# Kernel tuning notes

Measured on AMD Instinct MI355X. Metric: run time of the kernel, lower is better.

## Reference

```python
import jax, jax.numpy as jnp
import numpy as np

B, S, D, H, DFF = 2, 2048, 512, 8, 2048
DH = D // H
EPS = 1e-5


def setup_inputs() -> dict:
    key = jax.random.key(0)
    ks = jax.random.split(key, 12)
    g = lambda k, shape, s=0.02: jax.random.normal(k, shape, dtype=jnp.float32) * s
    x = jax.random.normal(ks[0], (B, S, D), dtype=jnp.float32)
    # additive causal mask: 0 on/below diag, -inf above
    neg = jnp.finfo(jnp.float32).min
    attn_mask = jnp.where(jnp.tril(jnp.ones((S, S), dtype=bool)), 0.0, neg).astype(jnp.float32)
    return {
        "x": x,
        "attn_mask": attn_mask,
        "Wq": g(ks[1], (D, D)), "bq": jnp.zeros((D,), jnp.float32),
        "Wk": g(ks[2], (D, D)), "bk": jnp.zeros((D,), jnp.float32),
        "Wv": g(ks[3], (D, D)), "bv": jnp.zeros((D,), jnp.float32),
        "Wo": g(ks[4], (D, D)), "bo": jnp.zeros((D,), jnp.float32),
        "head_alphas": jnp.ones((H,), jnp.float32),
        "ln1_g": jnp.ones((D,), jnp.float32), "ln1_b": jnp.zeros((D,), jnp.float32),
        "W1": g(ks[5], (DFF, D)), "b1": jnp.zeros((DFF,), jnp.float32),
        "W2": g(ks[6], (D, DFF)), "b2": jnp.zeros((D,), jnp.float32),
        "ln2_g": jnp.ones((D,), jnp.float32), "ln2_b": jnp.zeros((D,), jnp.float32),
    }


def _layer_norm(h, g, b):
    mu = jnp.mean(h, axis=-1, keepdims=True)
    var = jnp.mean((h - mu) ** 2, axis=-1, keepdims=True)
    return (h - mu) * jax.lax.rsqrt(var + EPS) * g + b


def reference(x, attn_mask, Wq, bq, Wk, bk, Wv, bv, Wo, bo, head_alphas,
              ln1_g, ln1_b, W1, b1, W2, b2, ln2_g, ln2_b):
    scale = jnp.sqrt(jnp.asarray(DH, dtype=x.dtype))
    # projections (torch Linear: x @ W.T + b)
    q = (x @ Wq.T + bq).reshape(B, S, H, DH).transpose(0, 2, 1, 3)  # bhsd
    k = (x @ Wk.T + bk).reshape(B, S, H, DH).transpose(0, 2, 1, 3)
    v = (x @ Wv.T + bv).reshape(B, S, H, DH).transpose(0, 2, 1, 3)
    attn = jnp.einsum('bhqd,bhkd->bhqk', q, k) / scale
    attn = attn + attn_mask  # broadcast [S,S] over batch/heads
    attn = jax.nn.softmax(attn, axis=-1)
    ctx = jnp.einsum('bhqk,bhkd->bhqd', attn, v)
    ctx = ctx * head_alphas[None, :, None, None]
    ctx = ctx.transpose(0, 2, 1, 3).reshape(B, S, D)
    attn_out = ctx @ Wo.T + bo
    # residual + LN
    h = _layer_norm(x + attn_out, ln1_g, ln1_b)
    # FFN (linear -> ReLU -> linear), residual + LN
    ff = jax.nn.relu(h @ W1.T + b1) @ W2.T + b2
    out = _layer_norm(h + ff, ln2_g, ln2_b)
    return out
```

## Files before the change

### kernel.cpp

```cpp
#include <hip/hip_runtime.h>
#include <hip/hip_bf16.h>
#include <math.h>

#define BB 2
#define SS 2048
#define DD 512
#define HH 8
#define DH 64
#define DFF 2048
#define MM (BB*SS)
#define EPS 1e-5f

typedef __attribute__((ext_vector_type(8))) short bf16x8;
typedef __attribute__((ext_vector_type(4))) float f32x4;

#define GL2LDS(g, l)                                                        \
    __builtin_amdgcn_global_load_lds(                                       \
        (const __attribute__((address_space(1))) void*)(unsigned long long)(g), \
        (__attribute__((address_space(3))) void*)(unsigned int)(unsigned long long)(l), \
        16, 0, 0)

struct Cvt7 {
    const float* s[7];
    unsigned short* d[7];
    unsigned off[8];
};

__global__ __launch_bounds__(256) void cvt_k(Cvt7 a)
{
    unsigned i = blockIdx.x * 256 + threadIdx.x;
    int seg = 0;
    #pragma unroll
    for (int t = 1; t < 7; ++t) seg += (i >= a.off[t]);
    unsigned li = i - a.off[seg];
    float4 v = ((const float4*)a.s[seg])[li];
    union { __hip_bfloat16 h[4]; uint2 u; } t;
    t.h[0] = __float2bfloat16(v.x);
    t.h[1] = __float2bfloat16(v.y);
    t.h[2] = __float2bfloat16(v.z);
    t.h[3] = __float2bfloat16(v.w);
    ((uint2*)a.d[seg])[li] = t.u;
}

template<int TM, int TN>
static __device__ __forceinline__ void gemm_core(
    __hip_bfloat16* As, __hip_bfloat16* Bs,
    const __hip_bfloat16* __restrict__ A, const __hip_bfloat16* __restrict__ Bw,
    const float* __restrict__ bias, const float* __restrict__ resid,
    void* __restrict__ Cout, int N_, int K_, int mode, float oscale)
{
    const int tid   = threadIdx.x;
    const int w     = tid >> 6;
    const int lane  = tid & 63;
    const int quad  = lane >> 4;
    const int col16 = lane & 15;
    const int m0 = blockIdx.y * TM;
    const int n0 = blockIdx.x * TN;
    constexpr int MI = TM / 32;
    constexpr int NJ = TN / 32;
    const int wm = (w >> 1) * (TM / 2);
    const int wn = (w & 1) * (TN / 2);

    const int srow = lane >> 3;
    const int scol = (lane & 7) * 8;
    constexpr int CH_A  = TM / 8;
    constexpr int CH_T  = (TM + TN) / 8;
    constexpr int TPW   = CH_T / 4;

    f32x4 acc[MI][NJ] = {};

    for (int k0 = 0; k0 < K_; k0 += 64) {
        __syncthreads();
        #pragma unroll
        for (int t = 0; t < TPW; ++t) {
            const int c = w * TPW + t;
            if (c < CH_A) {
                GL2LDS(A  + (size_t)(m0 + c*8 + srow) * K_ + k0 + scol,
                       (char*)As + c * 1024);
            } else {
                const int cb = c - CH_A;
                GL2LDS(Bw + (size_t)(n0 + cb*8 + srow) * K_ + k0 + scol,
                       (char*)Bs + cb * 1024);
            }
        }
        __syncthreads();

        #pragma unroll
        for (int kk = 0; kk < 64; kk += 32) {
            bf16x8 af[MI], bf[NJ];
            #pragma unroll
            for (int i = 0; i < MI; ++i)
                af[i] = *(const bf16x8*)(As + (wm + i*16 + col16) * 64 + kk + quad*8);
            #pragma unroll
            for (int j = 0; j < NJ; ++j)
                bf[j] = *(const bf16x8*)(Bs + (wn + j*16 + col16) * 64 + kk + quad*8);
            #pragma unroll
            for (int i = 0; i < MI; ++i)
                #pragma unroll
                for (int j = 0; j < NJ; ++j)
                    acc[i][j] = __builtin_amdgcn_mfma_f32_16x16x32_bf16(
                        af[i], bf[j], acc[i][j], 0, 0, 0);
        }
    }

    #pragma unroll
    for (int i = 0; i < MI; ++i) {
        #pragma unroll
        for (int r = 0; r < 4; ++r) {
            const int m = m0 + wm + i*16 + quad*4 + r;
            #pragma unroll
            for (int j = 0; j < NJ; ++j) {
                const int n = n0 + wn + j*16 + col16;
                float vv = acc[i][j][r] + bias[n];
                if (mode == 0) {
                    size_t idx = (size_t)m * N_ + n;
                    float* Cf = (float*)Cout;
                    if (resid) vv += resid[idx];
                    Cf[idx] = vv;
                } else if (mode == 3) {
                    ((__hip_bfloat16*)Cout)[(size_t)m * N_ + n] =
                        __float2bfloat16(fmaxf(vv, 0.f));
                } else {
                    const int b = m >> 11, s = m & (SS - 1);
                    const int hh = n >> 6, d = n & (DH - 1);
                    if (mode == 1)
                        ((__hip_bfloat16*)Cout)[(((size_t)(b*HH + hh))*SS + s)*DH + d] =
                            __float2bfloat16(vv * oscale);
                    else
                        ((__hip_bfloat16*)Cout)[(((size_t)(b*HH + hh))*DH + d)*SS + s] =
                            __float2bfloat16(vv);
                }
            }
        }
    }
}

__global__ __launch_bounds__(256) void gemm128_k(
    const __hip_bfloat16* __restrict__ A, const __hip_bfloat16* __restrict__ Bw,
    const float* __restrict__ bias, const float* __restrict__ resid,
    void* __restrict__ Cout, int N_, int K_, int mode, float oscale)
{
    __shared__ __hip_bfloat16 As[128*64];
    __shared__ __hip_bfloat16 Bs[128*64];
    gemm_core<128,128>(As, Bs, A, Bw, bias, resid, Cout, N_, K_, mode, oscale);
}

__global__ __launch_bounds__(256) void gemm64_k(
    const __hip_bfloat16* __restrict__ A, const __hip_bfloat16* __restrict__ Bw,
    const float* __restrict__ bias, const float* __restrict__ resid,
    void* __restrict__ Cout, int N_, int K_, int mode, float oscale)
{
    __shared__ __hip_bfloat16 As[64*64];
    __shared__ __hip_bfloat16 Bs[64*64];
    gemm_core<64,64>(As, Bs, A, Bw, bias, resid, Cout, N_, K_, mode, oscale);
}

__global__ __launch_bounds__(256) void qkv_mfma_k(
    const __hip_bfloat16* __restrict__ xb,
    const __hip_bfloat16* __restrict__ Wqb, const __hip_bfloat16* __restrict__ Wkb,
    const __hip_bfloat16* __restrict__ Wvb,
    const float* __restrict__ bq, const float* __restrict__ bk,
    const float* __restrict__ bv,
    __hip_bfloat16* __restrict__ qb, __hip_bfloat16* __restrict__ kb,
    __hip_bfloat16* __restrict__ vtb)
{
    __shared__ __hip_bfloat16 As[64*64];
    __shared__ __hip_bfloat16 Bs[64*64];
    const int z = blockIdx.z;
    const __hip_bfloat16* W = (z == 0) ? Wqb : (z == 1) ? Wkb : Wvb;
    const float* bia        = (z == 0) ? bq  : (z == 1) ? bk  : bv;
    void* dst               = (z == 0) ? (void*)qb : (z == 1) ? (void*)kb : (void*)vtb;
    const int mode          = (z == 2) ? 2 : 1;
    const float sc          = (z == 0) ? 0.125f : 1.0f;
    gemm_core<64,64>(As, Bs, xb, W, bia, nullptr, dst, DD, DD, mode, sc);
}

__global__ __launch_bounds__(256) void attn_mfma_k(
    const __hip_bfloat16* __restrict__ Q,
    const __hip_bfloat16* __restrict__ K,
    const __hip_bfloat16* __restrict__ VT,
    const float* __restrict__ halpha,
    __hip_bfloat16* __restrict__ ctx)
{
    const int w    = threadIdx.x >> 6;
    const int lane = threadIdx.x & 63;
    const int quad = lane >> 4;
    const int col  = lane & 15;
    const int bh   = blockIdx.x;
    const int b    = bh >> 3, h = bh & 7;
    const int qt   = gridDim.y - 1 - blockIdx.y;
    const int q0   = qt * 16;
    const int cd   = q0 >> 6;
    const int nchunk = cd + 1;

    const __hip_bfloat16* Qbh = Q  + (size_t)bh * SS * DH;
    const __hip_bfloat16* Kbh = K  + (size_t)bh * SS * DH;
    const __hip_bfloat16* Vbh = VT + (size_t)bh * DH * SS;

    __shared__ __hip_bfloat16 p_lds[4][2][64][8];
    __shared__ float o_lds[4][16][68];
    __shared__ float l_lds[4][16];

    bf16x8 qf0 = *(const bf16x8*)(Qbh + (size_t)(q0 + col) * DH + quad * 8);
    bf16x8 qf1 = *(const bf16x8*)(Qbh + (size_t)(q0 + col) * DH + 32 + quad * 8);

    f32x4 acc_o[4] = {};
    float lp[4] = {0.f, 0.f, 0.f, 0.f};

    for (int c = w; c < nchunk; c += 4) {
        const int k0 = c * 64;

        f32x4 sacc[4];
        #pragma unroll
        for (int ks = 0; ks < 4; ++ks) {
            const __hip_bfloat16* kp = Kbh + (size_t)(k0 + ks*16 + col) * DH + quad * 8;
            bf16x8 kb0 = *(const bf16x8*)(kp);
            bf16x8 kb1 = *(const bf16x8*)(kp + 32);
            f32x4 z = {};
            z = __builtin_amdgcn_mfma_f32_16x16x32_bf16(qf0, kb0, z, 0, 0, 0);
            z = __builtin_amdgcn_mfma_f32_16x16x32_bf16(qf1, kb1, z, 0, 0, 0);
            sacc[ks] = z;
        }

        float pv[4][4];
        if (c == cd) {
            #pragma unroll
            for (int ks = 0; ks < 4; ++ks) {
                int kg = k0 + ks*16 + col;
                #pragma unroll
                for (int r = 0; r < 4; ++r) {
                    int qg = q0 + quad*4 + r;
                    pv[ks][r] = (kg > qg) ? 0.f : __expf(sacc[ks][r]);
                }
            }
        } else {
            #pragma unroll
            for (int ks = 0; ks < 4; ++ks)
                #pragma unroll
                for (int r = 0; r < 4; ++r)
                    pv[ks][r] = __expf(sacc[ks][r]);
        }
        #pragma unroll
        for (int r = 0; r < 4; ++r)
            lp[r] += (pv[0][r] + pv[1][r]) + (pv[2][r] + pv[3][r]);

        #pragma unroll
        for (int ks = 0; ks < 4; ++ks) {
            int keyl = ks*16 + col;
            int kh = keyl >> 5;
            int lr = ((keyl >> 3) & 3) * 16;
            int j  = keyl & 7;
            #pragma unroll
            for (int r = 0; r < 4; ++r)
                p_lds[w][kh][lr + quad*4 + r][j] = __float2bfloat16(pv[ks][r]);
        }

        bf16x8 pa0 = *(const bf16x8*)&p_lds[w][0][lane][0];
        bf16x8 pa1 = *(const bf16x8*)&p_lds[w][1][lane][0];
        #pragma unroll
        for (int d = 0; d < 4; ++d) {
            const __hip_bfloat16* vp = Vbh + (size_t)(d*16 + col) * SS + k0 + quad * 8;
            bf16x8 vb0 = *(const bf16x8*)(vp);
            bf16x8 vb1 = *(const bf16x8*)(vp + 32);
            acc_o[d] = __builtin_amdgcn_mfma_f32_16x16x32_bf16(pa0, vb0, acc_o[d], 0, 0, 0);
            acc_o[d] = __builtin_amdgcn_mfma_f32_16x16x32_bf16(pa1, vb1, acc_o[d], 0, 0, 0);
        }
    }

    #pragma unroll
    for (int r = 0; r < 4; ++r) {
        float s_ = lp[r];
        #pragma unroll
        for (int o = 1; o < 16; o <<= 1) s_ += __shfl_xor(s_, o);
        lp[r] = s_;
    }

    if (col == 0) {
        #pragma unroll
        for (int r = 0; r < 4; ++r) l_lds[w][quad*4 + r] = lp[r];
    }
    #pragma unroll
    for (int d = 0; d < 4; ++d)
        #pragma unroll
        for (int r = 0; r < 4; ++r)
            o_lds[w][quad*4 + r][d*16 + col] = acc_o[d][r];
    __syncthreads();

    const float ha = halpha[h];
    #pragma unroll
    for (int r = 0; r < 4; ++r) {
        const int row = quad*4 + r;
        float L = (l_lds[0][row] + l_lds[1][row]) + (l_lds[2][row] + l_lds[3][row]);
        float val = (o_lds[0][row][w*16+col] + o_lds[1][row][w*16+col])
                  + (o_lds[2][row][w*16+col] + o_lds[3][row][w*16+col]);
        ctx[((size_t)(b*SS + q0 + row))*DD + h*64 + w*16 + col] =
            __float2bfloat16(val * ha / L);
    }
}

__global__ __launch_bounds__(256) void ln_k(
    const float* __restrict__ in, const float* __restrict__ g,
    const float* __restrict__ bta, float* __restrict__ out,
    __hip_bfloat16* __restrict__ outb)
{
    const int row = blockIdx.x;
    const float* p = in + (size_t)row * DD;
    const int t = threadIdx.x;
    float v0 = p[t], v1 = p[t + 256];
    __shared__ float red[256];
    red[t] = v0 + v1;
    __syncthreads();
    for (int o = 128; o > 0; o >>= 1) { if (t < o) red[t] += red[t + o]; __syncthreads(); }
    float mu = red[0] * (1.f / DD);
    __syncthreads();
    float d0 = v0 - mu, d1 = v1 - mu;
    red[t] = d0*d0 + d1*d1;
    __syncthreads();
    for (int o = 128; o > 0; o >>= 1) { if (t < o) red[t] += red[t + o]; __syncthreads(); }
    float rstd = rsqrtf(red[0] * (1.f / DD) + EPS);
    float o0 = d0 * rstd * g[t]       + bta[t];
    float o1 = d1 * rstd * g[t + 256] + bta[t + 256];
    out[(size_t)row * DD + t]       = o0;
    out[(size_t)row * DD + t + 256] = o1;
    if (outb) {
        outb[(size_t)row * DD + t]       = __float2bfloat16(o0);
        outb[(size_t)row * DD + t + 256] = __float2bfloat16(o1);
    }
}

extern "C" void kernel_launch(void* const* d_in, const int* in_sizes, int n_in,
                              void* d_out, int out_size, void* d_ws, size_t ws_size,
                              hipStream_t stream)
{
    const float* x    = (const float*)d_in[0];
    const float* Wq   = (const float*)d_in[2];
    const float* bq   = (const float*)d_in[3];
    const float* Wk   = (const float*)d_in[4];
    const float* bk   = (const float*)d_in[5];
    const float* Wv   = (const float*)d_in[6];
    const float* bv   = (const float*)d_in[7];
    const float* Wo   = (const float*)d_in[8];
    const float* bo   = (const float*)d_in[9];
    const float* hal  = (const float*)d_in[10];
    const float* ln1g = (const float*)d_in[11];
    const float* ln1b = (const float*)d_in[12];
    const float* W1   = (const float*)d_in[13];
    const float* b1   = (const float*)d_in[14];
    const float* W2   = (const float*)d_in[15];
    const float* b2   = (const float*)d_in[16];
    const float* ln2g = (const float*)d_in[17];
    const float* ln2b = (const float*)d_in[18];
    float* out = (float*)d_out;

    char* ws = (char*)d_ws;
    const size_t MB = 1ull << 20;
    __hip_bfloat16* Wqb = (__hip_bfloat16*)(ws);
    __hip_bfloat16* Wkb = (__hip_bfloat16*)(ws + MB/2);
    __hip_bfloat16* Wvb = (__hip_bfloat16*)(ws + MB);
    __hip_bfloat16* Wob = (__hip_bfloat16*)(ws + MB + MB/2);
    __hip_bfloat16* W1b = (__hip_bfloat16*)(ws + 2*MB);
    __hip_bfloat16* W2b = (__hip_bfloat16*)(ws + 4*MB);
    __hip_bfloat16* xb  = (__hip_bfloat16*)(ws + 6*MB);
    __hip_bfloat16* qb  = (__hip_bfloat16*)(ws + 10*MB);
    __hip_bfloat16* kb  = (__hip_bfloat16*)(ws + 14*MB);
    __hip_bfloat16* vtb = (__hip_bfloat16*)(ws + 18*MB);
    __hip_bfloat16* ctxb= (__hip_bfloat16*)(ws + 22*MB);
    float* h1  = (float*)(ws + 26*MB);
    float* h   = (float*)(ws + 34*MB);
    __hip_bfloat16* hb  = (__hip_bfloat16*)(ws + 42*MB);
    __hip_bfloat16* ff1b= (__hip_bfloat16*)(ws + 10*MB);
    float* f2  = (float*)(ws + 26*MB);

    dim3 blk(256);

    Cvt7 ca;
    ca.s[0] = x;  ca.d[0] = (unsigned short*)xb;
    ca.s[1] = Wq; ca.d[1] = (unsigned short*)Wqb;
    ca.s[2] = Wk; ca.d[2] = (unsigned short*)Wkb;
    ca.s[3] = Wv; ca.d[3] = (unsigned short*)Wvb;
    ca.s[4] = Wo; ca.d[4] = (unsigned short*)Wob;
    ca.s[5] = W1; ca.d[5] = (unsigned short*)W1b;
    ca.s[6] = W2; ca.d[6] = (unsigned short*)W2b;
    unsigned offs[8] = {0, 524288, 589824, 655360, 720896, 786432, 1048576, 1310720};
    for (int i = 0; i < 8; ++i) ca.off[i] = offs[i];
    cvt_k<<<dim3(5120), blk, 0, stream>>>(ca);

    qkv_mfma_k<<<dim3(DD/64, MM/64, 3), blk, 0, stream>>>(
        xb, Wqb, Wkb, Wvb, bq, bk, bv, qb, kb, vtb);

    attn_mfma_k<<<dim3(BB*HH, SS/16), blk, 0, stream>>>(qb, kb, vtb, hal, ctxb);

    gemm64_k<<<dim3(DD/64, MM/64), blk, 0, stream>>>(
        ctxb, Wob, bo, x, h1, DD, DD, 0, 1.0f);
    ln_k<<<dim3(MM), blk, 0, stream>>>(h1, ln1g, ln1b, h, hb);

    gemm128_k<<<dim3(DFF/128, MM/128), blk, 0, stream>>>(
        hb, W1b, b1, nullptr, ff1b, DFF, DD, 3, 1.0f);
    gemm64_k<<<dim3(DD/64, MM/64), blk, 0, stream>>>(
        ff1b, W2b, b2, h, f2, DD, DFF, 0, 1.0f);
    ln_k<<<dim3(MM), blk, 0, stream>>>(f2, ln2g, ln2b, out, nullptr);
}
```

Baseline: 275.3 us.

## Fuse QKV projection into one 128x128-tile GEMM and remap attention block order

Replaces the three-way z-indexed 64x64 QKV GEMM with a single kernel that treats Wq/Wk/Wv as one contiguous 1536x512 weight (relying on the bf16 conversion placing them adjacently) and uses 128x128 tiles with a 2x2 warp layout and 4x4 MFMA accumulators per warp. The epilogue scatters into the per-head Q, K and transposed V layouts with bias and query scaling. Larger tiles raise arithmetic intensity and cut the number of blocks, though the grid shrinks to 384 blocks. The attention kernel also permutes the batch/head index across blockIdx.x, likely to change how work spreads over the hardware.

```diff
diff --git a/kernel.cpp b/kernel.cpp
--- a/kernel.cpp
+++ b/kernel.cpp
@@ -155,24 +155,86 @@
     gemm_core<64,64>(As, Bs, A, Bw, bias, resid, Cout, N_, K_, mode, oscale);
 }
 
-__global__ __launch_bounds__(256) void qkv_mfma_k(
-    const __hip_bfloat16* __restrict__ xb,
-    const __hip_bfloat16* __restrict__ Wqb, const __hip_bfloat16* __restrict__ Wkb,
-    const __hip_bfloat16* __restrict__ Wvb,
+__global__ __launch_bounds__(256) void qkv_fused_k(
+    const __hip_bfloat16* __restrict__ A, const __hip_bfloat16* __restrict__ Wqkv,
     const float* __restrict__ bq, const float* __restrict__ bk,
     const float* __restrict__ bv,
     __hip_bfloat16* __restrict__ qb, __hip_bfloat16* __restrict__ kb,
     __hip_bfloat16* __restrict__ vtb)
 {
-    __shared__ __hip_bfloat16 As[64*64];
-    __shared__ __hip_bfloat16 Bs[64*64];
-    const int z = blockIdx.z;
-    const __hip_bfloat16* W = (z == 0) ? Wqb : (z == 1) ? Wkb : Wvb;
-    const float* bia        = (z == 0) ? bq  : (z == 1) ? bk  : bv;
-    void* dst               = (z == 0) ? (void*)qb : (z == 1) ? (void*)kb : (void*)vtb;
-    const int mode          = (z == 2) ? 2 : 1;
-    const float sc          = (z == 0) ? 0.125f : 1.0f;
-    gemm_core<64,64>(As, Bs, xb, W, bia, nullptr, dst, DD, DD, mode, sc);
+    __shared__ __hip_bfloat16 As[128*64];
+    __shared__ __hip_bfloat16 Bs[128*64];
+    const int tid   = threadIdx.x;
+    const int w     = tid >> 6;
+    const int lane  = tid & 63;
+    const int quad  = lane >> 4;
+    const int col16 = lane & 15;
+    const int m0 = blockIdx.y * 128;
+    const int n0 = blockIdx.x * 128;
+    const int wm = (w >> 1) * 64;
+    const int wn = (w & 1) * 64;
+    const int srow = lane >> 3;
+    const int scol = (lane & 7) * 8;
+
+    f32x4 acc[4][4] = {};
+
+    for (int k0 = 0; k0 < DD; k0 += 64) {
+        __syncthreads();
+        #pragma unroll
+        for (int t = 0; t < 8; ++t) {
+            const int c = w * 8 + t;
+            if (c < 16) {
+                GL2LDS(A    + (size_t)(m0 + c*8 + srow) * DD + k0 + scol,
+                       (char*)As + c * 1024);
+            } else {
+                const int cb = c - 16;
+                GL2LDS(Wqkv + (size_t)(n0 + cb*8 + srow) * DD + k0 + scol,
+                       (char*)Bs + cb * 1024);
+            }
+        }
+        __syncthreads();
+
+        #pragma unroll
+        for (int kk = 0; kk < 64; kk += 32) {
+            bf16x8 af[4], bf[4];
+            #pragma unroll
+            for (int i = 0; i < 4; ++i)
+                af[i] = *(const bf16x8*)(As + (wm + i*16 + col16) * 64 + kk + quad*8);
+            #pragma unroll
+            for (int j = 0; j < 4; ++j)
+                bf[j] = *(const bf16x8*)(Bs + (wn + j*16 + col16) * 64 + kk + quad*8);
+            #pragma unroll
+            for (int i = 0; i < 4; ++i)
+                #pragma unroll
+                for (int j = 0; j < 4; ++j)
+                    acc[i][j] = __builtin_amdgcn_mfma_f32_16x16x32_bf16(
+                        af[i], bf[j], acc[i][j], 0, 0, 0);
+        }
+    }
+
+    const int z = n0 >> 9;
+    const float* bias = (z == 0) ? bq : (z == 1) ? bk : bv;
+    __hip_bfloat16* dst = (z == 0) ? qb : (z == 1) ? kb : vtb;
+    const float sc = (z == 0) ? 0.125f : 1.0f;
+    #pragma unroll
+    for (int i = 0; i < 4; ++i) {
+        #pragma unroll
+        for (int r = 0; r < 4; ++r) {
+            const int m = m0 + wm + i*16 + quad*4 + r;
+            const int b = m >> 11, s = m & (SS - 1);
+            #pragma unroll
+            for (int j = 0; j < 4; ++j) {
+                const int n  = n0 + wn + j*16 + col16;
+                const int nn = n & 511;
+                const int hh = nn >> 6, d = nn & (DH - 1);
+                float vv = (acc[i][j][r] + bias[nn]) * sc;
+                if (z < 2)
+                    dst[(((size_t)(b*HH + hh))*SS + s)*DH + d] = __float2bfloat16(vv);
+                else
+                    dst[(((size_t)(b*HH + hh))*DH + d)*SS + s] = __float2bfloat16(vv);
+            }
+        }
+    }
 }
 
 __global__ __launch_bounds__(256) void attn_mfma_k(
@@ -186,7 +248,8 @@
     const int lane = threadIdx.x & 63;
     const int quad = lane >> 4;
     const int col  = lane & 15;
-    const int bh   = blockIdx.x;
+    const int xl   = blockIdx.x;
+    const int bh   = ((xl & 7) << 1) | (xl >> 3);
     const int b    = bh >> 3, h = bh & 7;
     const int qt   = gridDim.y - 1 - blockIdx.y;
     const int q0   = qt * 16;
@@ -385,8 +448,8 @@
     for (int i = 0; i < 8; ++i) ca.off[i] = offs[i];
     cvt_k<<<dim3(5120), blk, 0, stream>>>(ca);
 
-    qkv_mfma_k<<<dim3(DD/64, MM/64, 3), blk, 0, stream>>>(
-        xb, Wqb, Wkb, Wvb, bq, bk, bv, qb, kb, vtb);
+    qkv_fused_k<<<dim3((3*DD)/128, MM/128), blk, 0, stream>>>(
+        xb, Wqb, bq, bk, bv, qb, kb, vtb);
 
     attn_mfma_k<<<dim3(BB*HH, SS/16), blk, 0, stream>>>(qb, kb, vtb, hal, ctxb);
 
```

After: 280.0 us. About the same (+1.7%).
